# Optimization experiments

Measured on AMD Instinct MI355X. Metric: run time of the kernel, lower is better.

The kernel has to match this reference:

```python
import jax, jax.numpy as jnp
import numpy as np

B, N, D, E, K = 4, 4096, 768, 8, 2
H = 4 * D
LN_EPS = 1e-5


def setup_inputs() -> dict:
    key = jax.random.key(0)
    ks = jax.random.split(key, 9)
    s_d = 1.0 / np.sqrt(D)
    s_h = 1.0 / np.sqrt(H)
    return {
        "x": jax.random.normal(ks[0], (B, N, D), dtype=jnp.float32),
        "router_w": jax.random.normal(ks[1], (D, E), dtype=jnp.float32) * s_d,
        "router_b": jnp.zeros((E,), dtype=jnp.float32),
        "w1": jax.random.normal(ks[2], (E, D, H), dtype=jnp.float32) * s_d,
        "b1": jnp.zeros((E, H), dtype=jnp.float32),
        "w2": jax.random.normal(ks[3], (E, H, D), dtype=jnp.float32) * s_h,
        "b2": jnp.zeros((E, D), dtype=jnp.float32),
        "gamma": jnp.ones((D,), dtype=jnp.float32),
        "beta": jnp.zeros((D,), dtype=jnp.float32),
    }


def reference(x, router_w, router_b, w1, b1, w2, b2, gamma, beta):
    # Router logits and top-k gating (softmax over top-k values, in fp32)
    logits = jnp.einsum("bnd,de->bne", x, router_w) + router_b
    topv, topi = jax.lax.top_k(logits, K)                       # [B,N,K]
    w = jax.nn.softmax(topv.astype(jnp.float32), axis=-1).astype(x.dtype)
    # Per-token per-expert combine weight: [B,N,E]
    onehot = (topi[..., None] == jnp.arange(E)).astype(x.dtype)  # [B,N,K,E]
    we = jnp.einsum("bnk,bnke->bne", w, onehot)
    # Dense per-expert FFN, weighted combine (loop over small fixed E)
    out = jnp.zeros_like(x)
    for e in range(E):
        h = jax.nn.gelu(jnp.einsum("bnd,dh->bnh", x, w1[e]) + b1[e],
                        approximate=False)                      # exact GELU like torch
        y_e = jnp.einsum("bnh,hd->bnd", h, w2[e]) + b2[e]
        out = out + y_e * we[..., e:e + 1]
    # Residual + LayerNorm
    y = x + out
    mu = jnp.mean(y, axis=-1, keepdims=True)
    var = jnp.mean((y - mu) ** 2, axis=-1, keepdims=True)
    return (y - mu) * jax.lax.rsqrt(var + LN_EPS) * gamma + beta
```

## Files before the change

### kernel.cpp

```cpp
#include <hip/hip_runtime.h>
#include <hip/hip_bf16.h>
#include <math.h>

#define T_TOK 16384
#define DIM 768
#define NE 8
#define HID 3072
#define PADT 34816
#define NSLOT (T_TOK * 2)

typedef unsigned short u16;
typedef __attribute__((ext_vector_type(8))) short bf16x8;
typedef __attribute__((ext_vector_type(4))) float f32x4;

__device__ __forceinline__ u16 f2bf(float f) {
  union { float f; unsigned u; } v; v.f = f;
  unsigned r = v.u + 0x7FFF + ((v.u >> 16) & 1);
  return (u16)(r >> 16);
}

__device__ __forceinline__ float bf2f(u16 u) {
  union { unsigned u; float f; } v; v.u = ((unsigned)u) << 16; return v.f;
}

__device__ __forceinline__ void async16(void* lds, const void* g) {
  __builtin_amdgcn_global_load_lds((const __attribute__((address_space(1))) void*)g,
                                   (__attribute__((address_space(3))) void*)lds, 16, 0, 0);
}

__device__ __forceinline__ float gelu_f(float v) {
  float z = fabsf(v) * 0.70710678118f;
  float t = __builtin_amdgcn_rcpf(1.f + 0.3275911f * z);
  float p = t * (0.254829592f +
            t * (-0.284496736f +
            t * (1.421413741f +
            t * (-1.453152027f +
            t * 1.061405429f))));
  float e = __expf(-z * z);
  float erfz = fmaf(-p, e, 1.f);
  float s = copysignf(erfz, v);
  return 0.5f * v * (1.f + s);
}

__global__ __launch_bounds__(256) void transpose_cvt(const float* __restrict__ in,
                                                     u16* __restrict__ outp, int R, int C) {
  __shared__ float tile[32][33];
  int e = blockIdx.z;
  int c0 = blockIdx.x * 32, r0 = blockIdx.y * 32;
  int tx = threadIdx.x & 31, ty = threadIdx.x >> 5;
  const float* ip = in + (size_t)e * R * C;
  u16* op = outp + (size_t)e * R * C;
#pragma unroll
  for (int i = 0; i < 4; ++i)
    tile[ty + i * 8][tx] = ip[(size_t)(r0 + ty + i * 8) * C + c0 + tx];
  __syncthreads();
#pragma unroll
  for (int i = 0; i < 4; ++i)
    op[(size_t)(c0 + ty + i * 8) * R + r0 + tx] = f2bf(tile[tx][ty + i * 8]);
}

__global__ __launch_bounds__(256) void router_kernel(
    const float* __restrict__ x, const float* __restrict__ rw,
    const float* __restrict__ rb, int* __restrict__ idxb,
    float* __restrict__ wtb, u16* __restrict__ xb) {
  __shared__ float rwt[NE * DIM];
  for (int i = threadIdx.x; i < NE * DIM; i += 256) {
    int d = i >> 3, e = i & 7;
    rwt[e * DIM + d] = rw[i];
  }
  __syncthreads();
  int lane = threadIdx.x & 63, wv = threadIdx.x >> 6;
#pragma unroll 1
  for (int it = 0; it < 8; ++it) {
    int t = blockIdx.x * 32 + wv * 8 + it;
    const float4* xr = (const float4*)(x + (size_t)t * DIM);
    float4 xv[3];
#pragma unroll
    for (int i = 0; i < 3; ++i) xv[i] = xr[lane + i * 64];
    ushort4* xo = (ushort4*)(xb + (size_t)t * DIM);
#pragma unroll
    for (int i = 0; i < 3; ++i)
      xo[lane + i * 64] = make_ushort4(f2bf(xv[i].x), f2bf(xv[i].y), f2bf(xv[i].z), f2bf(xv[i].w));
    float acc[NE];
#pragma unroll
    for (int e = 0; e < NE; ++e) acc[e] = 0.f;
#pragma unroll
    for (int i = 0; i < 3; ++i) {
#pragma unroll
      for (int e = 0; e < NE; ++e) {
        float4 w4 = ((const float4*)(rwt + e * DIM))[lane + i * 64];
        acc[e] += xv[i].x * w4.x + xv[i].y * w4.y + xv[i].z * w4.z + xv[i].w * w4.w;
      }
    }
#pragma unroll
    for (int e = 0; e < NE; ++e)
      for (int off = 32; off; off >>= 1) acc[e] += __shfl_down(acc[e], off);
    if (lane == 0) {
      float lg[NE];
#pragma unroll
      for (int e = 0; e < NE; ++e) lg[e] = acc[e] + rb[e];
      int i0 = 0;
#pragma unroll
      for (int e = 1; e < NE; ++e) if (lg[e] > lg[i0]) i0 = e;
      int i1 = -1;
#pragma unroll
      for (int e = 0; e < NE; ++e)
        if (e != i0 && (i1 < 0 || lg[e] > lg[i1])) i1 = e;
      float ee = expf(lg[i1] - lg[i0]);
      float w0 = 1.f / (1.f + ee);
      float w1 = ee / (1.f + ee);
      idxb[t * 2] = i0; idxb[t * 2 + 1] = i1;
      wtb[t * 2] = w0; wtb[t * 2 + 1] = w1;
    }
  }
}

__global__ __launch_bounds__(256) void hist_kernel(const int* __restrict__ idxb,
                                                   int* __restrict__ whist) {
  int wv = threadIdx.x >> 6, lane = threadIdx.x & 63;
  int g = blockIdx.x * 4 + wv;
  int cnt = 0;
#pragma unroll
  for (int j = 0; j < 2; ++j) {
    int e = idxb[g * 128 + j * 64 + lane];
#pragma unroll
    for (int ex = 0; ex < NE; ++ex) {
      unsigned long long m = __ballot(e == ex);
      if (lane == ex) cnt += __popcll(m);
    }
  }
  if (lane < NE) whist[g * NE + lane] = cnt;
}

__global__ __launch_bounds__(256) void scan_kernel(const int* __restrict__ whist,
                                                   int* __restrict__ gbase,
                                                   int* __restrict__ offsets,
                                                   int* __restrict__ counts) {
  __shared__ int sgb[256 * NE];
  __shared__ int tot[NE], soff[NE + 1];
  int tid = threadIdx.x;
  if (tid < NE) {
    int run = 0;
    for (int g = 0; g < 256; ++g) { sgb[g * NE + tid] = run; run += whist[g * NE + tid]; }
    tot[tid] = run; counts[tid] = run;
  }
  __syncthreads();
  if (tid == 0) {
    int off = 0;
    for (int e = 0; e < NE; ++e) {
      soff[e] = off; offsets[e] = off;
      off += (tot[e] + 255) & ~255;
    }
    soff[NE] = off; offsets[NE] = off;
  }
  __syncthreads();
  for (int i = tid; i < 256 * NE; i += 256) gbase[i] = sgb[i] + soff[i & 7];
}

__global__ __launch_bounds__(256) void scatter_kernel(
    const int* __restrict__ idxb, const int* __restrict__ gbase,
    int* __restrict__ g_tok, int* __restrict__ pairpos) {
  int wv = threadIdx.x >> 6, lane = threadIdx.x & 63;
  int g = blockIdx.x * 4 + wv;
  int run = (lane < NE) ? gbase[g * NE + lane] : 0;
  unsigned long long ltm = (1ull << lane) - 1ull;
#pragma unroll
  for (int j = 0; j < 2; ++j) {
    int slot = g * 128 + j * 64 + lane;
    int e = idxb[slot];
    int myrank = 0;
#pragma unroll
    for (int ex = 0; ex < NE; ++ex) {
      unsigned long long m = __ballot(e == ex);
      int b = __shfl(run, ex);
      if (e == ex) myrank = b + __popcll(m & ltm);
      if (lane == ex) run += __popcll(m);
    }
    g_tok[myrank] = slot >> 1;
    pairpos[slot] = myrank;
  }
}


__global__ __launch_bounds__(512, 1) void gemm1_kernel(
    const u16* __restrict__ xb, const u16* __restrict__ w1t,
    const float* __restrict__ b1, const int* __restrict__ g_tok,
    const int* __restrict__ offsets, const int* __restrict__ counts,
    u16* __restrict__ hbuf, int g0) {
  const int g = g0 + blockIdx.y * 256;
  int e = -1;
#pragma unroll
  for (int i = 0; i < NE; ++i)
    if (g >= offsets[i] && g < offsets[i + 1]) e = i;
  if (e < 0) return;
  const int off = offsets[e], cnt = counts[e], r0 = g - off;
  if (r0 >= cnt) return;
  const int n0 = blockIdx.x * 128;

  __shared__ u16 As[3][256 * 64];
  __shared__ u16 Bs[3][128 * 64];

  const int tid = threadIdx.x;
  const int lane = tid & 63;
  const int w = tid >> 6;
  const int wm = w >> 1;
  const int wn = w & 1;
  const int src = ((lane & 7) ^ (lane >> 3)) * 8;
  const int lrow = w * 8 + (lane >> 3);

  const u16* ap[4];
  const u16* bp[2];
#pragma unroll
  for (int i = 0; i < 4; ++i) {
    int r = r0 + i * 64 + lrow;
    int rr = r < cnt ? r : cnt - 1;
    ap[i] = xb + (size_t)g_tok[off + rr] * DIM + src;
  }
#pragma unroll
  for (int i = 0; i < 2; ++i)
    bp[i] = w1t + ((size_t)e * HID + n0 + i * 64 + lrow) * DIM + src;

  f32x4 acc[4][4];
#pragma unroll
  for (int i = 0; i < 4; ++i)
#pragma unroll
    for (int j = 0; j < 4; ++j) acc[i][j] = (f32x4){0.f, 0.f, 0.f, 0.f};

  const int NT = DIM / 64;
  auto stage = [&](int buf, int kt) {
#pragma unroll
    for (int i = 0; i < 4; ++i)
      async16(&As[buf][(i * 64 + w * 8) * 64], ap[i] + kt * 64);
#pragma unroll
    for (int i = 0; i < 2; ++i)
      async16(&Bs[buf][(i * 64 + w * 8) * 64], bp[i] + kt * 64);
  };
  stage(0, 0);
  stage(1, 1);
  asm volatile("s_waitcnt vmcnt(6)" ::: "memory");
  __builtin_amdgcn_s_barrier();

#pragma unroll 1
  for (int t = 0; t < NT; ++t) {
    const int bc = t % 3;
    if (t + 2 < NT) stage((t + 2) % 3, t + 2);
    bf16x8 bfr[4][2];
#pragma unroll
    for (int nj = 0; nj < 4; ++nj)
#pragma unroll
      for (int kk = 0; kk < 2; ++kk)
        bfr[nj][kk] = *(const bf16x8*)&Bs[bc][(wn * 64 + nj * 16 + (lane & 15)) * 64 +
                                             (((kk * 4 + (lane >> 4)) ^ (lane & 7)) * 8)];
    __builtin_amdgcn_s_setprio(1);
#pragma unroll
    for (int mi = 0; mi < 4; ++mi) {
      bf16x8 af[2];
#pragma unroll
      for (int kk = 0; kk < 2; ++kk)
        af[kk] = *(const bf16x8*)&As[bc][(wm * 64 + mi * 16 + (lane & 15)) * 64 +
                                         (((kk * 4 + (lane >> 4)) ^ (lane & 7)) * 8)];
#pragma unroll
      for (int nj = 0; nj < 4; ++nj)
#pragma unroll
        for (int kk = 0; kk < 2; ++kk)
          acc[mi][nj] = __builtin_amdgcn_mfma_f32_16x16x32_bf16(af[kk], bfr[nj][kk],
                                                                acc[mi][nj], 0, 0, 0);
    }
    __builtin_amdgcn_s_setprio(0);
    if (t + 1 < NT) {
      if (t + 2 < NT) asm volatile("s_waitcnt vmcnt(6)" ::: "memory");
      else            asm volatile("s_waitcnt vmcnt(0)" ::: "memory");
      __builtin_amdgcn_s_barrier();
    }
  }

#pragma unroll
  for (int mi = 0; mi < 4; ++mi)
#pragma unroll
    for (int nj = 0; nj < 4; ++nj) {
      int col = n0 + wn * 64 + nj * 16 + (lane & 15);
      float bias = b1[e * HID + col];
#pragma unroll
      for (int rg = 0; rg < 4; ++rg) {
        int rloc = wm * 64 + mi * 16 + (lane >> 4) * 4 + rg;
        if (r0 + rloc < cnt)
          hbuf[(size_t)(g - g0 + rloc) * HID + col] = f2bf(gelu_f(acc[mi][nj][rg] + bias));
      }
    }
}

__global__ __launch_bounds__(512, 1) void gemm2_kernel(
    const u16* __restrict__ hbuf, const u16* __restrict__ w2t,
    const float* __restrict__ b2, const int* __restrict__ offsets,
    const int* __restrict__ counts, u16* __restrict__ ygb, int g0) {
  const int g = g0 + blockIdx.y * 256;
  int e = -1;
#pragma unroll
  for (int i = 0; i < NE; ++i)
    if (g >= offsets[i] && g < offsets[i + 1]) e = i;
  if (e < 0) return;
  const int off = offsets[e], cnt = counts[e], r0 = g - off;
  if (r0 >= cnt) return;
  const int n0 = blockIdx.x * 128;

  __shared__ u16 As[3][256 * 64];
  __shared__ u16 Bs[3][128 * 64];

  const int tid = threadIdx.x;
  const int lane = tid & 63;
  const int w = tid >> 6;
  const int wm = w >> 1;
  const int wn = w & 1;
  const int src = ((lane & 7) ^ (lane >> 3)) * 8;
  const int lrow = w * 8 + (lane >> 3);

  const u16* ap[4];
  const u16* bp[2];
#pragma unroll
  for (int i = 0; i < 4; ++i) {
    int r = r0 + i * 64 + lrow;
    int rr = r < cnt ? r : cnt - 1;
    ap[i] = hbuf + (size_t)(off + rr - g0) * HID + src;
  }
#pragma unroll
  for (int i = 0; i < 2; ++i)
    bp[i] = w2t + ((size_t)e * DIM + n0 + i * 64 + lrow) * HID + src;

  f32x4 acc[4][4];
#pragma unroll
  for (int i = 0; i < 4; ++i)
#pragma unroll
    for (int j = 0; j < 4; ++j) acc[i][j] = (f32x4){0.f, 0.f, 0.f, 0.f};

  const int NT = HID / 64;
  auto stage = [&](int buf, int kt) {
#pragma unroll
    for (int i = 0; i < 4; ++i)
      async16(&As[buf][(i * 64 + w * 8) * 64], ap[i] + kt * 64);
#pragma unroll
    for (int i = 0; i < 2; ++i)
      async16(&Bs[buf][(i * 64 + w * 8) * 64], bp[i] + kt * 64);
  };
  stage(0, 0);
  stage(1, 1);
  asm volatile("s_waitcnt vmcnt(6)" ::: "memory");
  __builtin_amdgcn_s_barrier();

#pragma unroll 1
  for (int t = 0; t < NT; ++t) {
    const int bc = t % 3;
    if (t + 2 < NT) stage((t + 2) % 3, t + 2);
    bf16x8 bfr[4][2];
#pragma unroll
    for (int nj = 0; nj < 4; ++nj)
#pragma unroll
      for (int kk = 0; kk < 2; ++kk)
        bfr[nj][kk] = *(const bf16x8*)&Bs[bc][(wn * 64 + nj * 16 + (lane & 15)) * 64 +
                                             (((kk * 4 + (lane >> 4)) ^ (lane & 7)) * 8)];
    __builtin_amdgcn_s_setprio(1);
#pragma unroll
    for (int mi = 0; mi < 4; ++mi) {
      bf16x8 af[2];
#pragma unroll
      for (int kk = 0; kk < 2; ++kk)
        af[kk] = *(const bf16x8*)&As[bc][(wm * 64 + mi * 16 + (lane & 15)) * 64 +
                                         (((kk * 4 + (lane >> 4)) ^ (lane & 7)) * 8)];
#pragma unroll
      for (int nj = 0; nj < 4; ++nj)
#pragma unroll
        for (int kk = 0; kk < 2; ++kk)
          acc[mi][nj] = __builtin_amdgcn_mfma_f32_16x16x32_bf16(af[kk], bfr[nj][kk],
                                                                acc[mi][nj], 0, 0, 0);
    }
    __builtin_amdgcn_s_setprio(0);
    if (t + 1 < NT) {
      if (t + 2 < NT) asm volatile("s_waitcnt vmcnt(6)" ::: "memory");
      else            asm volatile("s_waitcnt vmcnt(0)" ::: "memory");
      __builtin_amdgcn_s_barrier();
    }
  }

#pragma unroll
  for (int mi = 0; mi < 4; ++mi)
#pragma unroll
    for (int nj = 0; nj < 4; ++nj) {
      int col = n0 + wn * 64 + nj * 16 + (lane & 15);
      float bias = b2[e * DIM + col];
#pragma unroll
      for (int rg = 0; rg < 4; ++rg) {
        int rloc = wm * 64 + mi * 16 + (lane >> 4) * 4 + rg;
        if (r0 + rloc < cnt)
          ygb[(size_t)(g + rloc) * DIM + col] = f2bf(acc[mi][nj][rg] + bias);
      }
    }
}

__global__ __launch_bounds__(256) void combine_ln_kernel(
    const float* __restrict__ x, const u16* __restrict__ ygb,
    const int* __restrict__ pairpos, const float* __restrict__ wtb,
    const float* __restrict__ gamma, const float* __restrict__ beta,
    float* __restrict__ out) {
  int t = blockIdx.x;
  int p0 = pairpos[t * 2], p1 = pairpos[t * 2 + 1];
  float w0 = wtb[t * 2], w1 = wtb[t * 2 + 1];
  const float* xr = x + (size_t)t * DIM;
  const u16* y0 = ygb + (size_t)p0 * DIM;
  const u16* y1 = ygb + (size_t)p1 * DIM;
  float y[3];
  float s = 0.f, s2 = 0.f;
#pragma unroll
  for (int i = 0; i < 3; ++i) {
    int d = threadIdx.x + i * 256;
    float v = xr[d] + w0 * bf2f(y0[d]) + w1 * bf2f(y1[d]);
    y[i] = v; s += v; s2 += v * v;
  }
  for (int o = 32; o; o >>= 1) { s += __shfl_down(s, o); s2 += __shfl_down(s2, o); }
  __shared__ float red[8];
  int lane = threadIdx.x & 63, wv = threadIdx.x >> 6;
  if (lane == 0) { red[wv] = s; red[4 + wv] = s2; }
  __syncthreads();
  s = red[0] + red[1] + red[2] + red[3];
  s2 = red[4] + red[5] + red[6] + red[7];
  float mu = s * (1.f / DIM);
  float var = s2 * (1.f / DIM) - mu * mu;
  float inv = 1.f / sqrtf(var + 1e-5f);
#pragma unroll
  for (int i = 0; i < 3; ++i) {
    int d = threadIdx.x + i * 256;
    out[(size_t)t * DIM + d] = (y[i] - mu) * inv * gamma[d] + beta[d];
  }
}

extern "C" void kernel_launch(void* const* d_in, const int* in_sizes, int n_in,
                              void* d_out, int out_size, void* d_ws, size_t ws_size,
                              hipStream_t stream) {
  const float* x = (const float*)d_in[0];
  const float* rw = (const float*)d_in[1];
  const float* rb = (const float*)d_in[2];
  const float* w1 = (const float*)d_in[3];
  const float* b1 = (const float*)d_in[4];
  const float* w2 = (const float*)d_in[5];
  const float* b2 = (const float*)d_in[6];
  const float* gamma = (const float*)d_in[7];
  const float* beta = (const float*)d_in[8];
  float* out = (float*)d_out;

  char* p = (char*)d_ws;
  size_t o = 0;
  auto take = [&](size_t b) { void* q = (void*)(p + o); o += (b + 255) & ~((size_t)255); return q; };
  u16* xb = (u16*)take((size_t)T_TOK * DIM * 2);
  u16* w1t = (u16*)take((size_t)NE * HID * DIM * 2);
  u16* w2t = (u16*)take((size_t)NE * DIM * HID * 2);
  u16* ygb = (u16*)take((size_t)PADT * DIM * 2);
  int* g_tok = (int*)take((size_t)PADT * 4);
  int* pairpos = (int*)take((size_t)NSLOT * 4);
  int* idxb = (int*)take((size_t)NSLOT * 4);
  float* wtb = (float*)take((size_t)NSLOT * 4);
  int* whist = (int*)take((size_t)256 * NE * 4);
  int* gbase = (int*)take((size_t)256 * NE * 4);
  int* counts = (int*)take(64);
  int* offsets = (int*)take(64);
  (void)in_sizes; (void)n_in; (void)out_size;

  if (o + 256 > ws_size) return;
  size_t rem = ws_size - o;
  int chunk = (int)(rem / ((size_t)HID * 2));
  if (chunk > PADT) chunk = PADT;
  chunk &= ~255;
  if (chunk < 256) return;
  u16* hbuf = (u16*)take((size_t)chunk * HID * 2);

  router_kernel<<<512, 256, 0, stream>>>(x, rw, rb, idxb, wtb, xb);
  transpose_cvt<<<dim3(HID / 32, DIM / 32, NE), 256, 0, stream>>>(w1, w1t, DIM, HID);
  transpose_cvt<<<dim3(DIM / 32, HID / 32, NE), 256, 0, stream>>>(w2, w2t, HID, DIM);
  hist_kernel<<<64, 256, 0, stream>>>(idxb, whist);
  scan_kernel<<<1, 256, 0, stream>>>(whist, gbase, offsets, counts);
  scatter_kernel<<<64, 256, 0, stream>>>(idxb, gbase, g_tok, pairpos);
  for (int g0 = 0; g0 < PADT; g0 += chunk) {
    int nrow = chunk / 256;
    gemm1_kernel<<<dim3(HID / 128, nrow), 512, 0, stream>>>(
        xb, w1t, b1, g_tok, offsets, counts, hbuf, g0);
    gemm2_kernel<<<dim3(DIM / 128, nrow), 512, 0, stream>>>(
        hbuf, w2t, b2, offsets, counts, ygb, g0);
  }
  combine_ln_kernel<<<T_TOK, 256, 0, stream>>>(x, ygb, pairpos, wtb, gamma, beta, out);
}
```

Measured before the change: 785.6 us.

## Enlarge grouped GEMM tiles to 256x256 with interleaved double-buffered loads

Both expert GEMM kernels move from 256x128 output tiles to 256x256 tiles. Eight waves are arranged 2x4, each computing 128x64, and the K-loop is split into four quarter phases. Shared memory goes from a triple buffer to a double buffer, and the global-to-LDS async loads for the next stages are spread across those phases, with barriers between them. The goal is higher arithmetic intensity per loaded byte and overlap of loads with MFMA work, at the cost of more accumulator registers, more barriers, and fewer blocks (for GEMM2 only 3 column tiles per row block).

```diff
diff --git a/kernel.cpp b/kernel.cpp
--- a/kernel.cpp
+++ b/kernel.cpp
@@ -195,94 +195,119 @@
   if (e < 0) return;
   const int off = offsets[e], cnt = counts[e], r0 = g - off;
   if (r0 >= cnt) return;
-  const int n0 = blockIdx.x * 128;
-
-  __shared__ u16 As[3][256 * 64];
-  __shared__ u16 Bs[3][128 * 64];
+  const int n0 = blockIdx.x * 256;
+
+  __shared__ u16 Asm[2][256 * 64];
+  __shared__ u16 Bsm[2][256 * 64];
 
   const int tid = threadIdx.x;
   const int lane = tid & 63;
   const int w = tid >> 6;
-  const int wm = w >> 1;
-  const int wn = w & 1;
-  const int src = ((lane & 7) ^ (lane >> 3)) * 8;
-  const int lrow = w * 8 + (lane >> 3);
-
-  const u16* ap[4];
-  const u16* bp[2];
-#pragma unroll
-  for (int i = 0; i < 4; ++i) {
-    int r = r0 + i * 64 + lrow;
+  const int wm = w >> 2;
+  const int wn = w & 3;
+  const int l3 = lane >> 3;
+  const int scol = ((lane & 7) ^ l3) * 8;
+  const int fr = lane & 15;
+  const int kq = lane >> 4;
+  const int x7 = lane & 7;
+
+  const u16* apq[4];
+#pragma unroll
+  for (int q = 0; q < 4; ++q) {
+    int r = r0 + (w >> 2) * 128 + q * 32 + (w & 3) * 8 + l3;
     int rr = r < cnt ? r : cnt - 1;
-    ap[i] = xb + (size_t)g_tok[off + rr] * DIM + src;
-  }
-#pragma unroll
-  for (int i = 0; i < 2; ++i)
-    bp[i] = w1t + ((size_t)e * HID + n0 + i * 64 + lrow) * DIM + src;
-
-  f32x4 acc[4][4];
-#pragma unroll
-  for (int i = 0; i < 4; ++i)
+    apq[q] = xb + (size_t)g_tok[off + rr] * DIM + scol;
+  }
+  const u16* bpq[4];
+#pragma unroll
+  for (int b = 0; b < 4; ++b)
+    bpq[b] = w1t + ((size_t)e * HID + n0 + b * 64 + w * 8 + l3) * DIM + scol;
+
+  const int adst = ((w >> 2) * 128 + (w & 3) * 8) * 64;
+  const int bdst = (w * 8) * 64;
+  auto stageA = [&](int buf, int kt, int q) {
+    async16(&Asm[buf][adst + q * 32 * 64], apq[q] + kt * 64);
+  };
+  auto stageB = [&](int buf, int kt, int b) {
+    async16(&Bsm[buf][bdst + b * 64 * 64], bpq[b] + kt * 64);
+  };
+
+  f32x4 acc[8][4];
+#pragma unroll
+  for (int i = 0; i < 8; ++i)
 #pragma unroll
     for (int j = 0; j < 4; ++j) acc[i][j] = (f32x4){0.f, 0.f, 0.f, 0.f};
 
   const int NT = DIM / 64;
-  auto stage = [&](int buf, int kt) {
-#pragma unroll
-    for (int i = 0; i < 4; ++i)
-      async16(&As[buf][(i * 64 + w * 8) * 64], ap[i] + kt * 64);
-#pragma unroll
-    for (int i = 0; i < 2; ++i)
-      async16(&Bs[buf][(i * 64 + w * 8) * 64], bp[i] + kt * 64);
-  };
-  stage(0, 0);
-  stage(1, 1);
+#pragma unroll
+  for (int q = 0; q < 4; ++q) stageA(0, 0, q);
+#pragma unroll
+  for (int b = 0; b < 4; ++b) stageB(0, 0, b);
+#pragma unroll
+  for (int q = 0; q < 3; ++q) stageA(1, 1, q);
+#pragma unroll
+  for (int b = 0; b < 3; ++b) stageB(1, 1, b);
   asm volatile("s_waitcnt vmcnt(6)" ::: "memory");
   __builtin_amdgcn_s_barrier();
 
 #pragma unroll 1
-  for (int t = 0; t < NT; ++t) {
-    const int bc = t % 3;
-    if (t + 2 < NT) stage((t + 2) % 3, t + 2);
+  for (int i = 0; i < NT; ++i) {
+    const int p = i & 1;
     bf16x8 bfr[4][2];
 #pragma unroll
-    for (int nj = 0; nj < 4; ++nj)
-#pragma unroll
-      for (int kk = 0; kk < 2; ++kk)
-        bfr[nj][kk] = *(const bf16x8*)&Bs[bc][(wn * 64 + nj * 16 + (lane & 15)) * 64 +
-                                             (((kk * 4 + (lane >> 4)) ^ (lane & 7)) * 8)];
-    __builtin_amdgcn_s_setprio(1);
-#pragma unroll
-    for (int mi = 0; mi < 4; ++mi) {
-      bf16x8 af[2];
-#pragma unroll
-      for (int kk = 0; kk < 2; ++kk)
-        af[kk] = *(const bf16x8*)&As[bc][(wm * 64 + mi * 16 + (lane & 15)) * 64 +
-                                         (((kk * 4 + (lane >> 4)) ^ (lane & 7)) * 8)];
-#pragma unroll
-      for (int nj = 0; nj < 4; ++nj)
+    for (int q = 0; q < 4; ++q) {
+      bf16x8 af[2][2];
+#pragma unroll
+      for (int m2 = 0; m2 < 2; ++m2)
 #pragma unroll
         for (int kk = 0; kk < 2; ++kk)
-          acc[mi][nj] = __builtin_amdgcn_mfma_f32_16x16x32_bf16(af[kk], bfr[nj][kk],
-                                                                acc[mi][nj], 0, 0, 0);
-    }
-    __builtin_amdgcn_s_setprio(0);
-    if (t + 1 < NT) {
-      if (t + 2 < NT) asm volatile("s_waitcnt vmcnt(6)" ::: "memory");
-      else            asm volatile("s_waitcnt vmcnt(0)" ::: "memory");
+          af[m2][kk] = *(const bf16x8*)&Asm[p][(wm * 128 + (q * 2 + m2) * 16 + fr) * 64 +
+                                              (((kk * 4 + kq) ^ x7) * 8)];
+      if (q == 0) {
+#pragma unroll
+        for (int nj = 0; nj < 4; ++nj)
+#pragma unroll
+          for (int kk = 0; kk < 2; ++kk)
+            bfr[nj][kk] = *(const bf16x8*)&Bsm[p][(wn * 64 + nj * 16 + fr) * 64 +
+                                                  (((kk * 4 + kq) ^ x7) * 8)];
+        if (i + 1 < NT) { stageA(p ^ 1, i + 1, 3); stageB(p ^ 1, i + 1, 3); }
+      } else if (q == 1) {
+        if (i + 2 < NT) stageA(p, i + 2, 0);
+      } else if (q == 2) {
+        if (i + 2 < NT) { stageA(p, i + 2, 1); stageB(p, i + 2, 0); }
+      } else {
+        if (i + 2 < NT) { stageA(p, i + 2, 2); stageB(p, i + 2, 1); stageB(p, i + 2, 2); }
+      }
       __builtin_amdgcn_s_barrier();
-    }
-  }
-
-#pragma unroll
-  for (int mi = 0; mi < 4; ++mi)
+      asm volatile("s_waitcnt lgkmcnt(0)" ::: "memory");
+      __builtin_amdgcn_sched_barrier(0);
+      __builtin_amdgcn_s_setprio(1);
+#pragma unroll
+      for (int m2 = 0; m2 < 2; ++m2)
+#pragma unroll
+        for (int nj = 0; nj < 4; ++nj)
+#pragma unroll
+          for (int kk = 0; kk < 2; ++kk)
+            acc[q * 2 + m2][nj] = __builtin_amdgcn_mfma_f32_16x16x32_bf16(
+                af[m2][kk], bfr[nj][kk], acc[q * 2 + m2][nj], 0, 0, 0);
+      __builtin_amdgcn_s_setprio(0);
+      if (q == 3) {
+        if (i + 2 < NT) asm volatile("s_waitcnt vmcnt(6)" ::: "memory");
+        else            asm volatile("s_waitcnt vmcnt(0)" ::: "memory");
+      }
+      __builtin_amdgcn_s_barrier();
+    }
+  }
+
+#pragma unroll
+  for (int mi = 0; mi < 8; ++mi)
 #pragma unroll
     for (int nj = 0; nj < 4; ++nj) {
-      int col = n0 + wn * 64 + nj * 16 + (lane & 15);
+      int col = n0 + wn * 64 + nj * 16 + fr;
       float bias = b1[e * HID + col];
 #pragma unroll
       for (int rg = 0; rg < 4; ++rg) {
-        int rloc = wm * 64 + mi * 16 + (lane >> 4) * 4 + rg;
+        int rloc = wm * 128 + mi * 16 + kq * 4 + rg;
         if (r0 + rloc < cnt)
           hbuf[(size_t)(g - g0 + rloc) * HID + col] = f2bf(gelu_f(acc[mi][nj][rg] + bias));
       }
@@ -301,94 +326,119 @@
   if (e < 0) return;
   const int off = offsets[e], cnt = counts[e], r0 = g - off;
   if (r0 >= cnt) return;
-  const int n0 = blockIdx.x * 128;
-
-  __shared__ u16 As[3][256 * 64];
-  __shared__ u16 Bs[3][128 * 64];
+  const int n0 = blockIdx.x * 256;
+
+  __shared__ u16 Asm[2][256 * 64];
+  __shared__ u16 Bsm[2][256 * 64];
 
   const int tid = threadIdx.x;
   const int lane = tid & 63;
   const int w = tid >> 6;
-  const int wm = w >> 1;
-  const int wn = w & 1;
-  const int src = ((lane & 7) ^ (lane >> 3)) * 8;
-  const int lrow = w * 8 + (lane >> 3);
-
-  const u16* ap[4];
-  const u16* bp[2];
-#pragma unroll
-  for (int i = 0; i < 4; ++i) {
-    int r = r0 + i * 64 + lrow;
+  const int wm = w >> 2;
+  const int wn = w & 3;
+  const int l3 = lane >> 3;
+  const int scol = ((lane & 7) ^ l3) * 8;
+  const int fr = lane & 15;
+  const int kq = lane >> 4;
+  const int x7 = lane & 7;
+
+  const u16* apq[4];
+#pragma unroll
+  for (int q = 0; q < 4; ++q) {
+    int r = r0 + (w >> 2) * 128 + q * 32 + (w & 3) * 8 + l3;
     int rr = r < cnt ? r : cnt - 1;
-    ap[i] = hbuf + (size_t)(off + rr - g0) * HID + src;
-  }
-#pragma unroll
-  for (int i = 0; i < 2; ++i)
-    bp[i] = w2t + ((size_t)e * DIM + n0 + i * 64 + lrow) * HID + src;
-
-  f32x4 acc[4][4];
-#pragma unroll
-  for (int i = 0; i < 4; ++i)
+    apq[q] = hbuf + (size_t)(off + rr - g0) * HID + scol;
+  }
+  const u16* bpq[4];
+#pragma unroll
+  for (int b = 0; b < 4; ++b)
+    bpq[b] = w2t + ((size_t)e * DIM + n0 + b * 64 + w * 8 + l3) * HID + scol;
+
+  const int adst = ((w >> 2) * 128 + (w & 3) * 8) * 64;
+  const int bdst = (w * 8) * 64;
+  auto stageA = [&](int buf, int kt, int q) {
+    async16(&Asm[buf][adst + q * 32 * 64], apq[q] + kt * 64);
+  };
+  auto stageB = [&](int buf, int kt, int b) {
+    async16(&Bsm[buf][bdst + b * 64 * 64], bpq[b] + kt * 64);
+  };
+
+  f32x4 acc[8][4];
+#pragma unroll
+  for (int i = 0; i < 8; ++i)
 #pragma unroll
     for (int j = 0; j < 4; ++j) acc[i][j] = (f32x4){0.f, 0.f, 0.f, 0.f};
 
   const int NT = HID / 64;
-  auto stage = [&](int buf, int kt) {
-#pragma unroll
-    for (int i = 0; i < 4; ++i)
-      async16(&As[buf][(i * 64 + w * 8) * 64], ap[i] + kt * 64);
-#pragma unroll
-    for (int i = 0; i < 2; ++i)
-      async16(&Bs[buf][(i * 64 + w * 8) * 64], bp[i] + kt * 64);
-  };
-  stage(0, 0);
-  stage(1, 1);
+#pragma unroll
+  for (int q = 0; q < 4; ++q) stageA(0, 0, q);
+#pragma unroll
+  for (int b = 0; b < 4; ++b) stageB(0, 0, b);
+#pragma unroll
+  for (int q = 0; q < 3; ++q) stageA(1, 1, q);
+#pragma unroll
+  for (int b = 0; b < 3; ++b) stageB(1, 1, b);
   asm volatile("s_waitcnt vmcnt(6)" ::: "memory");
   __builtin_amdgcn_s_barrier();
 
 #pragma unroll 1
-  for (int t = 0; t < NT; ++t) {
-    const int bc = t % 3;
-    if (t + 2 < NT) stage((t + 2) % 3, t + 2);
+  for (int i = 0; i < NT; ++i) {
+    const int p = i & 1;
     bf16x8 bfr[4][2];
 #pragma unroll
-    for (int nj = 0; nj < 4; ++nj)
-#pragma unroll
-      for (int kk = 0; kk < 2; ++kk)
-        bfr[nj][kk] = *(const bf16x8*)&Bs[bc][(wn * 64 + nj * 16 + (lane & 15)) * 64 +
-                                             (((kk * 4 + (lane >> 4)) ^ (lane & 7)) * 8)];
-    __builtin_amdgcn_s_setprio(1);
-#pragma unroll
-    for (int mi = 0; mi < 4; ++mi) {
-      bf16x8 af[2];
-#pragma unroll
-      for (int kk = 0; kk < 2; ++kk)
-        af[kk] = *(const bf16x8*)&As[bc][(wm * 64 + mi * 16 + (lane & 15)) * 64 +
-                                         (((kk * 4 + (lane >> 4)) ^ (lane & 7)) * 8)];
-#pragma unroll
-      for (int nj = 0; nj < 4; ++nj)
+    for (int q = 0; q < 4; ++q) {
+      bf16x8 af[2][2];
+#pragma unroll
+      for (int m2 = 0; m2 < 2; ++m2)
 #pragma unroll
         for (int kk = 0; kk < 2; ++kk)
-          acc[mi][nj] = __builtin_amdgcn_mfma_f32_16x16x32_bf16(af[kk], bfr[nj][kk],
-                                                                acc[mi][nj], 0, 0, 0);
-    }
-    __builtin_amdgcn_s_setprio(0);
-    if (t + 1 < NT) {
-      if (t + 2 < NT) asm volatile("s_waitcnt vmcnt(6)" ::: "memory");
-      else            asm volatile("s_waitcnt vmcnt(0)" ::: "memory");
+          af[m2][kk] = *(const bf16x8*)&Asm[p][(wm * 128 + (q * 2 + m2) * 16 + fr) * 64 +
+                                              (((kk * 4 + kq) ^ x7) * 8)];
+      if (q == 0) {
+#pragma unroll
+        for (int nj = 0; nj < 4; ++nj)
+#pragma unroll
+          for (int kk = 0; kk < 2; ++kk)
+            bfr[nj][kk] = *(const bf16x8*)&Bsm[p][(wn * 64 + nj * 16 + fr) * 64 +
+                                                  (((kk * 4 + kq) ^ x7) * 8)];
+        if (i + 1 < NT) { stageA(p ^ 1, i + 1, 3); stageB(p ^ 1, i + 1, 3); }
+      } else if (q == 1) {
+        if (i + 2 < NT) stageA(p, i + 2, 0);
+      } else if (q == 2) {
+        if (i + 2 < NT) { stageA(p, i + 2, 1); stageB(p, i + 2, 0); }
+      } else {
+        if (i + 2 < NT) { stageA(p, i + 2, 2); stageB(p, i + 2, 1); stageB(p, i + 2, 2); }
+      }
       __builtin_amdgcn_s_barrier();
-    }
-  }
-
-#pragma unroll
-  for (int mi = 0; mi < 4; ++mi)
+      asm volatile("s_waitcnt lgkmcnt(0)" ::: "memory");
+      __builtin_amdgcn_sched_barrier(0);
+      __builtin_amdgcn_s_setprio(1);
+#pragma unroll
+      for (int m2 = 0; m2 < 2; ++m2)
+#pragma unroll
+        for (int nj = 0; nj < 4; ++nj)
+#pragma unroll
+          for (int kk = 0; kk < 2; ++kk)
+            acc[q * 2 + m2][nj] = __builtin_amdgcn_mfma_f32_16x16x32_bf16(
+                af[m2][kk], bfr[nj][kk], acc[q * 2 + m2][nj], 0, 0, 0);
+      __builtin_amdgcn_s_setprio(0);
+      if (q == 3) {
+        if (i + 2 < NT) asm volatile("s_waitcnt vmcnt(6)" ::: "memory");
+        else            asm volatile("s_waitcnt vmcnt(0)" ::: "memory");
+      }
+      __builtin_amdgcn_s_barrier();
+    }
+  }
+
+#pragma unroll
+  for (int mi = 0; mi < 8; ++mi)
 #pragma unroll
     for (int nj = 0; nj < 4; ++nj) {
-      int col = n0 + wn * 64 + nj * 16 + (lane & 15);
+      int col = n0 + wn * 64 + nj * 16 + fr;
       float bias = b2[e * DIM + col];
 #pragma unroll
       for (int rg = 0; rg < 4; ++rg) {
-        int rloc = wm * 64 + mi * 16 + (lane >> 4) * 4 + rg;
+        int rloc = wm * 128 + mi * 16 + kq * 4 + rg;
         if (r0 + rloc < cnt)
           ygb[(size_t)(g + rloc) * DIM + col] = f2bf(acc[mi][nj][rg] + bias);
       }
@@ -478,9 +528,9 @@
   scatter_kernel<<<64, 256, 0, stream>>>(idxb, gbase, g_tok, pairpos);
   for (int g0 = 0; g0 < PADT; g0 += chunk) {
     int nrow = chunk / 256;
-    gemm1_kernel<<<dim3(HID / 128, nrow), 512, 0, stream>>>(
+    gemm1_kernel<<<dim3(HID / 256, nrow), 512, 0, stream>>>(
         xb, w1t, b1, g_tok, offsets, counts, hbuf, g0);
-    gemm2_kernel<<<dim3(DIM / 128, nrow), 512, 0, stream>>>(
+    gemm2_kernel<<<dim3(DIM / 256, nrow), 512, 0, stream>>>(
         hbuf, w2t, b2, offsets, counts, ygb, g0);
   }
   combine_ln_kernel<<<T_TOK, 256, 0, stream>>>(x, ygb, pairpos, wtb, gamma, beta, out);
```

Result: slower. 822.7 us (+4.7%).
